# Optimization experiments

Hardware: AMD Instinct MI355X
Metric: run time of the kernel (lower is better)

The kernel has to match this reference:

```python
import jax, jax.numpy as jnp
import numpy as np
import math

H = 32      # num attention heads
KV = 8      # num key/value heads
D = 64      # head dim
ROPE_BASE = 10000.0


def _rope_cos_sin(seq_len, dtype):
    inv_freq = 1.0 / (ROPE_BASE ** (jnp.arange(0, D, 2, dtype=jnp.float32) / D))
    t = jnp.arange(seq_len, dtype=jnp.float32)
    freqs = jnp.einsum('i,j->ij', t, inv_freq)          # [S, D/2]
    emb = jnp.concatenate([freqs, freqs], axis=-1)       # [S, D]
    return jnp.cos(emb).astype(dtype)[None, None], jnp.sin(emb).astype(dtype)[None, None]


def _rotate_half(x):
    x1, x2 = x[..., : D // 2], x[..., D // 2:]
    return jnp.concatenate([-x2, x1], axis=-1)


def setup_inputs() -> dict:
    key = jax.random.key(0)
    ks = jax.random.split(key, 5)
    B, S, Hid = 1, 2048, 2048
    hidden_states = jax.random.normal(ks[0], (B, S, Hid), dtype=jnp.float32)
    Wq = jax.random.normal(ks[1], (Hid, H * D), dtype=jnp.float32) * (1.0 / math.sqrt(Hid))
    Wk = jax.random.normal(ks[2], (Hid, KV * D), dtype=jnp.float32) * (1.0 / math.sqrt(Hid))
    Wv = jax.random.normal(ks[3], (Hid, KV * D), dtype=jnp.float32) * (1.0 / math.sqrt(Hid))
    Wo = jax.random.normal(ks[4], (H * D, Hid), dtype=jnp.float32) * (1.0 / math.sqrt(H * D))
    # additive causal mask
    causal = jnp.tril(jnp.ones((S, S), dtype=bool))
    attention_mask = jnp.where(causal, 0.0, -1e9).astype(jnp.float32)[None, None]
    return {"hidden_states": hidden_states, "Wq": Wq, "Wk": Wk, "Wv": Wv,
            "Wo": Wo, "attention_mask": attention_mask}


def reference(hidden_states, Wq, Wk, Wv, Wo, attention_mask):
    B, S, _ = hidden_states.shape
    groups = H // KV
    # projections -> [B, heads, S, D]
    q = (hidden_states @ Wq).reshape(B, S, H, D).transpose(0, 2, 1, 3)
    k = (hidden_states @ Wk).reshape(B, S, KV, D).transpose(0, 2, 1, 3)
    v = (hidden_states @ Wv).reshape(B, S, KV, D).transpose(0, 2, 1, 3)
    # RoPE
    cos, sin = _rope_cos_sin(S, q.dtype)
    q = q * cos + _rotate_half(q) * sin
    k = k * cos + _rotate_half(k) * sin
    # GQA head expansion (repeat_interleave along head axis)
    k = jnp.repeat(k, groups, axis=1)
    v = jnp.repeat(v, groups, axis=1)
    # scaled dot-product attention (eager)
    scores = jnp.einsum('bhqd,bhkd->bhqk', q, k) / math.sqrt(D)
    scores = scores + attention_mask
    probs = jax.nn.softmax(scores.astype(jnp.float32), axis=-1).astype(q.dtype)
    attn = jnp.einsum('bhqk,bhkd->bhqd', probs, v)
    attn = attn.transpose(0, 2, 1, 3).reshape(B, S, H * D)
    return attn @ Wo
```

## Files before the change

### kernel.cpp

```cpp
#include <hip/hip_runtime.h>
#include <hip/hip_bf16.h>
#include <math.h>

#define S_LEN 2048
#define HID   2048
#define NH    32
#define NKV   8
#define HD    64
#define KVW   (NKV * HD)

typedef __attribute__((ext_vector_type(8))) short bf16x8;
typedef __attribute__((ext_vector_type(4))) float f32x4;
typedef unsigned short u16;

__device__ __forceinline__ u16 f2bf(float f) {
    return (u16)((__builtin_bit_cast(unsigned, f) + 0x8000u) >> 16);
}
__device__ __forceinline__ float bf2f(u16 v) {
    unsigned u = ((unsigned)v) << 16;
    return __builtin_bit_cast(float, u);
}
__device__ __forceinline__ unsigned pack2bf(float a, float b) {
    unsigned ua = __builtin_bit_cast(unsigned, a) + 0x8000u;
    unsigned ub = __builtin_bit_cast(unsigned, b) + 0x8000u;
    return (ua >> 16) | (ub & 0xFFFF0000u);
}
__device__ __forceinline__ void stage16(const u16* g, u16* lds_base) {
    __builtin_amdgcn_global_load_lds((const __attribute__((address_space(1))) void*)g,
                                     (__attribute__((address_space(3))) void*)lds_base, 16, 0, 0);
}

__global__ __launch_bounds__(256) void cvt_bf16x8_kernel(const float* __restrict__ X,
                                                         u16* __restrict__ Y, int n8) {
    int i = blockIdx.x * 256 + threadIdx.x;
    if (i >= n8) return;
    const float4* p = (const float4*)(X + (size_t)i * 8);
    float4 a = p[0], b = p[1];
    uint4 o;
    o.x = pack2bf(a.x, a.y);
    o.y = pack2bf(a.z, a.w);
    o.z = pack2bf(b.x, b.y);
    o.w = pack2bf(b.z, b.w);
    *(uint4*)(Y + (size_t)i * 8) = o;
}

__global__ __launch_bounds__(256) void transpose_cvt4(const float* __restrict__ Wq,
                                                      const float* __restrict__ Wk,
                                                      const float* __restrict__ Wv,
                                                      const float* __restrict__ Wo,
                                                      u16* __restrict__ WqkvT,
                                                      u16* __restrict__ WoT) {
    const float* X; u16* Y; int C;
    const int z = blockIdx.z;
    if (z == 0)      { X = Wq; Y = WqkvT;                        C = HID; }
    else if (z == 1) { X = Wo; Y = WoT;                          C = HID; }
    else if (z == 2) { X = Wk; Y = WqkvT + (size_t)2048 * HID;   C = KVW; }
    else             { X = Wv; Y = WqkvT + (size_t)2560 * HID;   C = KVW; }
    const int c0 = blockIdx.x * 32, r0 = blockIdx.y * 32;
    if (c0 >= C) return;
    __shared__ float T[32][33];
    const int tx = threadIdx.x & 31, ty = threadIdx.x >> 5;
#pragma unroll
    for (int i = 0; i < 4; i++)
        T[ty + 8 * i][tx] = X[(size_t)(r0 + ty + 8 * i) * C + c0 + tx];
    __syncthreads();
#pragma unroll
    for (int i = 0; i < 4; i++)
        Y[(size_t)(c0 + ty + 8 * i) * HID + r0 + tx] = f2bf(T[tx][ty + 8 * i]);
}

template <int EPI>
__global__ __launch_bounds__(256, 4) void gemm_bf16(const u16* __restrict__ A,
                                                    const u16* __restrict__ Bt,
                                                    float* __restrict__ C,
                                                    u16* __restrict__ Qh,
                                                    u16* __restrict__ Kh,
                                                    u16* __restrict__ Vt,
                                                    int K) {
    __shared__ u16 As[2][128 * 64];
    __shared__ u16 Bs[2][64 * 64];

    const int t = threadIdx.x;
    const int w = t >> 6, lane = t & 63;
    const int qd = lane >> 4, r = lane & 15;
    const int wm = w >> 1, wn = w & 1;
    const int bm = blockIdx.y * 128, bn = blockIdx.x * 64;
    const bool kblk = (EPI == 1) && (bn >= 2048) && (bn < 2560);

    f32x4 acc[4][2];
#pragma unroll
    for (int i = 0; i < 4; i++)
#pragma unroll
        for (int j = 0; j < 2; j++) {
            acc[i][j][0] = 0.f; acc[i][j][1] = 0.f; acc[i][j][2] = 0.f; acc[i][j][3] = 0.f;
        }

    auto stageA = [&](int k0, u16* dstA) {
#pragma unroll
        for (int rd = 0; rd < 4; rd++) {
            int chunk = rd * 4 + w;
            int tt = chunk >> 1, ss = chunk & 1;
            const u16* g = A + (size_t)(bm + tt * 16 + r) * K + k0 + ss * 32 + qd * 8;
            stage16(g, dstA + chunk * 512);
        }
    };
    auto stageB = [&](int k0, u16* dstB) {
#pragma unroll
        for (int rd = 0; rd < 2; rd++) {
            int chunk = rd * 4 + w;
            int tt = chunk >> 1, ss = chunk & 1;
            const u16* g = Bt + (size_t)(bn + tt * 16 + r) * K + k0 + ss * 32 + qd * 8;
            stage16(g, dstB + chunk * 512);
        }
    };

    stageA(0, As[0]);
    stageB(0, Bs[0]);
    __syncthreads();
    int cur = 0;

    for (int k0 = 0; k0 < K; k0 += 64) {
        if (k0 + 64 < K) {
            stageA(k0 + 64, As[cur ^ 1]);
            stageB(k0 + 64, Bs[cur ^ 1]);
        }

#pragma unroll
        for (int ss = 0; ss < 2; ss++) {
            bf16x8 af[4], bfr[2];
#pragma unroll
            for (int i = 0; i < 4; i++)
                af[i] = *(const bf16x8*)&As[cur][((wm * 4 + i) * 2 + ss) * 512 + lane * 8];
#pragma unroll
            for (int j = 0; j < 2; j++) {
                int tile = kblk ? (wn + 2 * j) : (wn * 2 + j);
                bfr[j] = *(const bf16x8*)&Bs[cur][(tile * 2 + ss) * 512 + lane * 8];
            }
#pragma unroll
            for (int i = 0; i < 4; i++)
#pragma unroll
                for (int j = 0; j < 2; j++)
                    acc[i][j] = __builtin_amdgcn_mfma_f32_16x16x32_bf16(af[i], bfr[j], acc[i][j], 0, 0, 0);
        }

        __syncthreads();
        cur ^= 1;
    }

    const int row0 = bm + wm * 64;
    if (EPI == 0) {
#pragma unroll
        for (int i = 0; i < 4; i++)
#pragma unroll
            for (int j = 0; j < 2; j++)
#pragma unroll
                for (int reg = 0; reg < 4; reg++)
                    C[(size_t)(row0 + i * 16 + qd * 4 + reg) * HID + bn + wn * 32 + j * 16 + r] =
                        acc[i][j][reg];
    } else if (bn < 2048) {
#pragma unroll
        for (int i = 0; i < 4; i++)
#pragma unroll
            for (int j = 0; j < 2; j++)
#pragma unroll
                for (int reg = 0; reg < 4; reg++)
                    Qh[(size_t)(row0 + i * 16 + qd * 4 + reg) * HID + bn + wn * 32 + j * 16 + r] =
                        f2bf(acc[i][j][reg]);
    } else if (kblk) {
        const int c0 = wn * 16 + r;
        const float inv = __expf(-(float)c0 * 0.2878231366242596f);
#pragma unroll
        for (int i = 0; i < 4; i++)
#pragma unroll
            for (int reg = 0; reg < 4; reg++) {
                int srow = row0 + i * 16 + qd * 4 + reg;
                float ang = (float)srow * inv;
                float cs = cosf(ang), sn = sinf(ang);
                float k1 = acc[i][0][reg], k2 = acc[i][1][reg];
                size_t o = (size_t)srow * KVW + (bn - 2048) + c0;
                Kh[o]      = f2bf(k1 * cs - k2 * sn);
                Kh[o + 32] = f2bf(k2 * cs + k1 * sn);
            }
    } else {
#pragma unroll
        for (int i = 0; i < 4; i++)
#pragma unroll
            for (int j = 0; j < 2; j++) {
                int nrel = (bn - 2560) + wn * 32 + j * 16 + r;
                int m0 = row0 + i * 16 + qd * 4;
                ushort4 v;
                v.x = f2bf(acc[i][j][0]); v.y = f2bf(acc[i][j][1]);
                v.z = f2bf(acc[i][j][2]); v.w = f2bf(acc[i][j][3]);
                *(ushort4*)(Vt + (size_t)nrel * S_LEN + m0) = v;
            }
    }
}

__global__ __launch_bounds__(512, 6) void attn_mfma(const u16* __restrict__ Qh,
                                                    const u16* __restrict__ K,
                                                    const u16* __restrict__ Vt,
                                                    u16* __restrict__ O) {
    __shared__ u16 Kbuf[2][4096];
    __shared__ u16 Vbuf[4096];
    __shared__ u16 P_lds[8][16][72];

    const int w    = threadIdx.x >> 6;
    const int lane = threadIdx.x & 63;
    const int qd   = lane >> 4;
    const int r    = lane & 15;
    const int qb   = 15 - (int)blockIdx.x;
    const int h    = blockIdx.y;
    const int kvh  = h >> 2;
    const int q0w  = qb * 128 + w * 16;

    const u16* qrow = Qh + (size_t)(q0w + r) * (NH * HD) + h * HD;
    bf16x8 qlo = *(const bf16x8*)(qrow + qd * 8);
    bf16x8 qhi = *(const bf16x8*)(qrow + 32 + qd * 8);
    float y1[8], y2[8];
    const float spos = (float)(q0w + r);
    const float LN1E4_OVER_32 = 0.2878231366242596f;
#pragma unroll
    for (int i = 0; i < 8; i++) {
        int jj = qd * 8 + i;
        float x1 = bf2f((u16)qlo[i]);
        float x2 = bf2f((u16)qhi[i]);
        float inv = __expf(-(float)jj * LN1E4_OVER_32);
        float ang = spos * inv;
        float c = cosf(ang), sn = sinf(ang);
        y1[i] = (x1 * c - x2 * sn) * 0.125f;
        y2[i] = (x2 * c + x1 * sn) * 0.125f;
    }
    bf16x8 qfrag[2];
    {
        union { unsigned u[4]; bf16x8 v; } a, b;
#pragma unroll
        for (int i = 0; i < 4; i++) {
            a.u[i] = pack2bf(y1[2 * i], y1[2 * i + 1]);
            b.u[i] = pack2bf(y2[2 * i], y2[2 * i + 1]);
        }
        qfrag[0] = a.v; qfrag[1] = b.v;
    }

    bf16x8 ones;
    {
        union { u16 s[8]; bf16x8 v; } u;
#pragma unroll
        for (int i = 0; i < 8; i++) u.s[i] = 0x3F80;
        ones = u.v;
    }

    f32x4 oacc[4];
    f32x4 lacc;
#pragma unroll
    for (int i = 0; i < 4; i++) { oacc[i][0]=0.f; oacc[i][1]=0.f; oacc[i][2]=0.f; oacc[i][3]=0.f; }
    lacc[0]=0.f; lacc[1]=0.f; lacc[2]=0.f; lacc[3]=0.f;

    const int ktmax = 2 * qb + 1;

#define STAGE_K(kt_, buf_)                                                        \
    {                                                                             \
        const u16* g = K + (size_t)((kt_) * 64 + (w >> 1) * 16 + r) * KVW         \
                         + kvh * HD + (w & 1) * 32 + qd * 8;                      \
        stage16(g, &Kbuf[buf_][w * 512]);                                         \
    }
#define STAGE_V(kt_)                                                              \
    {                                                                             \
        const u16* g = Vt + (size_t)(kvh * HD + (w >> 1) * 16 + r) * S_LEN        \
                          + (kt_) * 64 + (w & 1) * 32 + qd * 8;                   \
        stage16(g, &Vbuf[w * 512]);                                               \
    }

    STAGE_K(0, 0);
    __syncthreads();
    int cur = 0;

    for (int kt = 0; kt <= ktmax; kt++) {
        STAGE_V(kt);
        if (kt < ktmax) STAGE_K(kt + 1, cur ^ 1);

        f32x4 s[4];
#pragma unroll
        for (int nt = 0; nt < 4; nt++) {
            bf16x8 kf0 = *(const bf16x8*)&Kbuf[cur][(nt * 2 + 0) * 512 + lane * 8];
            bf16x8 kf1 = *(const bf16x8*)&Kbuf[cur][(nt * 2 + 1) * 512 + lane * 8];
            f32x4 z; z[0]=0.f; z[1]=0.f; z[2]=0.f; z[3]=0.f;
            z = __builtin_amdgcn_mfma_f32_16x16x32_bf16(qfrag[0], kf0, z, 0, 0, 0);
            s[nt] = __builtin_amdgcn_mfma_f32_16x16x32_bf16(qfrag[1], kf1, z, 0, 0, 0);
        }

        if (kt * 64 + 63 > q0w) {
#pragma unroll
            for (int nt = 0; nt < 4; nt++) {
                int key = kt * 64 + nt * 16 + r;
#pragma unroll
                for (int reg = 0; reg < 4; reg++) {
                    int qg = q0w + qd * 4 + reg;
                    if (key > qg) s[nt][reg] = -1e30f;
                }
            }
        }

#pragma unroll
        for (int nt = 0; nt < 4; nt++)
#pragma unroll
            for (int reg = 0; reg < 4; reg++)
                P_lds[w][qd * 4 + reg][nt * 16 + r] = f2bf(__expf(s[nt][reg]));

        __syncthreads();

#pragma unroll
        for (int c = 0; c < 2; c++) {
            bf16x8 pf = *(const bf16x8*)&P_lds[w][r][c * 32 + qd * 8];
            lacc = __builtin_amdgcn_mfma_f32_16x16x32_bf16(pf, ones, lacc, 0, 0, 0);
#pragma unroll
            for (int ntd = 0; ntd < 4; ntd++) {
                bf16x8 vf = *(const bf16x8*)&Vbuf[(ntd * 2 + c) * 512 + lane * 8];
                oacc[ntd] = __builtin_amdgcn_mfma_f32_16x16x32_bf16(pf, vf, oacc[ntd], 0, 0, 0);
            }
        }

        __syncthreads();
        cur ^= 1;
    }
#undef STAGE_K
#undef STAGE_V

    float rl[4];
#pragma unroll
    for (int reg = 0; reg < 4; reg++) rl[reg] = 1.f / lacc[reg];
#pragma unroll
    for (int ntd = 0; ntd < 4; ntd++)
#pragma unroll
        for (int reg = 0; reg < 4; reg++)
            O[(size_t)(q0w + qd * 4 + reg) * (NH * HD) + h * HD + ntd * 16 + r] =
                f2bf(oacc[ntd][reg] * rl[reg]);
}

extern "C" void kernel_launch(void* const* d_in, const int* in_sizes, int n_in,
                              void* d_out, int out_size, void* d_ws, size_t ws_size,
                              hipStream_t stream) {
    const float* hidden = (const float*)d_in[0];
    const float* Wq = (const float*)d_in[1];
    const float* Wk = (const float*)d_in[2];
    const float* Wv = (const float*)d_in[3];
    const float* Wo = (const float*)d_in[4];
    float* out = (float*)d_out;

    char* ws = (char*)d_ws;
    const size_t MB = 1024 * 1024;
    u16* Hh     = (u16*)(ws + 0 * MB);
    u16* WqkvT  = (u16*)(ws + 8 * MB);
    u16* WoT    = (u16*)(ws + 20 * MB);
    u16* Qh     = (u16*)(ws + 28 * MB);
    u16* Kh     = (u16*)(ws + 36 * MB);
    u16* Vt     = (u16*)(ws + 38 * MB);
    u16* Ob     = WqkvT;

    cvt_bf16x8_kernel<<<(S_LEN * HID / 8 + 255) / 256, 256, 0, stream>>>(hidden, Hh, S_LEN * HID / 8);
    transpose_cvt4<<<dim3(HID / 32, HID / 32, 4), 256, 0, stream>>>(Wq, Wk, Wv, Wo, WqkvT, WoT);

    gemm_bf16<1><<<dim3(3072 / 64, S_LEN / 128), 256, 0, stream>>>(Hh, WqkvT, nullptr, Qh, Kh, Vt, HID);

    attn_mfma<<<dim3(S_LEN / 128, NH), 512, 0, stream>>>(Qh, Kh, Vt, Ob);

    gemm_bf16<0><<<dim3(HID / 64, S_LEN / 128), 256, 0, stream>>>(Ob, WoT, out, nullptr, nullptr, nullptr, HID);
}
```

Baseline: 286.1 us.

## Widen GEMM tiles to 128x128 and double-buffer V in attention

The bf16 GEMM moves from 128x64 tiles with 4 waves to 128x128 tiles with 8 waves. A and B are now staged together, one 16-row strip per wave, and the RoPE epilogue remaps so each block covers two K heads. This raises reuse of the A tile, but it halves the number of blocks on a 256-CU GPU, which risks load imbalance and lower occupancy. In attention, V is now double-buffered and prefetched alongside K, and the barrier between the per-wave P write and P read is removed, cutting one workgroup sync per key tile.

After: 285.0 us. Within noise of the previous version (-0.4%).

```diff
diff --git a/kernel.cpp b/kernel.cpp
--- a/kernel.cpp
+++ b/kernel.cpp
@@ -70,7 +70,7 @@
 }
 
 template <int EPI>
-__global__ __launch_bounds__(256, 4) void gemm_bf16(const u16* __restrict__ A,
+__global__ __launch_bounds__(512, 4) void gemm_bf16(const u16* __restrict__ A,
                                                     const u16* __restrict__ Bt,
                                                     float* __restrict__ C,
                                                     u16* __restrict__ Qh,
@@ -78,13 +78,13 @@
                                                     u16* __restrict__ Vt,
                                                     int K) {
     __shared__ u16 As[2][128 * 64];
-    __shared__ u16 Bs[2][64 * 64];
+    __shared__ u16 Bs[2][128 * 64];
 
     const int t = threadIdx.x;
     const int w = t >> 6, lane = t & 63;
     const int qd = lane >> 4, r = lane & 15;
-    const int wm = w >> 1, wn = w & 1;
-    const int bm = blockIdx.y * 128, bn = blockIdx.x * 64;
+    const int wm = w >> 2, wn = w & 3;
+    const int bm = blockIdx.y * 128, bn = blockIdx.x * 128;
     const bool kblk = (EPI == 1) && (bn >= 2048) && (bn < 2560);
 
     f32x4 acc[4][2];
@@ -95,35 +95,23 @@
             acc[i][j][0] = 0.f; acc[i][j][1] = 0.f; acc[i][j][2] = 0.f; acc[i][j][3] = 0.f;
         }
 
-    auto stageA = [&](int k0, u16* dstA) {
-#pragma unroll
-        for (int rd = 0; rd < 4; rd++) {
-            int chunk = rd * 4 + w;
-            int tt = chunk >> 1, ss = chunk & 1;
-            const u16* g = A + (size_t)(bm + tt * 16 + r) * K + k0 + ss * 32 + qd * 8;
-            stage16(g, dstA + chunk * 512);
+    auto stageAB = [&](int k0, u16* dstA, u16* dstB) {
+#pragma unroll
+        for (int rd = 0; rd < 2; rd++) {
+            const u16* ga = A + (size_t)(bm + w * 16 + r) * K + k0 + rd * 32 + qd * 8;
+            stage16(ga, dstA + (w * 2 + rd) * 512);
+            const u16* gb = Bt + (size_t)(bn + w * 16 + r) * K + k0 + rd * 32 + qd * 8;
+            stage16(gb, dstB + (w * 2 + rd) * 512);
         }
     };
-    auto stageB = [&](int k0, u16* dstB) {
-#pragma unroll
-        for (int rd = 0; rd < 2; rd++) {
-            int chunk = rd * 4 + w;
-            int tt = chunk >> 1, ss = chunk & 1;
-            const u16* g = Bt + (size_t)(bn + tt * 16 + r) * K + k0 + ss * 32 + qd * 8;
-            stage16(g, dstB + chunk * 512);
-        }
-    };
-
-    stageA(0, As[0]);
-    stageB(0, Bs[0]);
+
+    stageAB(0, As[0], Bs[0]);
     __syncthreads();
     int cur = 0;
 
     for (int k0 = 0; k0 < K; k0 += 64) {
-        if (k0 + 64 < K) {
-            stageA(k0 + 64, As[cur ^ 1]);
-            stageB(k0 + 64, Bs[cur ^ 1]);
-        }
+        if (k0 + 64 < K)
+            stageAB(k0 + 64, As[cur ^ 1], Bs[cur ^ 1]);
 
 #pragma unroll
         for (int ss = 0; ss < 2; ss++) {
@@ -133,7 +121,7 @@
                 af[i] = *(const bf16x8*)&As[cur][((wm * 4 + i) * 2 + ss) * 512 + lane * 8];
 #pragma unroll
             for (int j = 0; j < 2; j++) {
-                int tile = kblk ? (wn + 2 * j) : (wn * 2 + j);
+                int tile = kblk ? ((wn >> 1) * 4 + (wn & 1) + 2 * j) : (wn * 2 + j);
                 bfr[j] = *(const bf16x8*)&Bs[cur][(tile * 2 + ss) * 512 + lane * 8];
             }
 #pragma unroll
@@ -167,7 +155,8 @@
                     Qh[(size_t)(row0 + i * 16 + qd * 4 + reg) * HID + bn + wn * 32 + j * 16 + r] =
                         f2bf(acc[i][j][reg]);
     } else if (kblk) {
-        const int c0 = wn * 16 + r;
+        const int c0 = (wn & 1) * 16 + r;
+        const int hb = (bn - 2048) + (wn >> 1) * 64;
         const float inv = __expf(-(float)c0 * 0.2878231366242596f);
 #pragma unroll
         for (int i = 0; i < 4; i++)
@@ -177,7 +166,7 @@
                 float ang = (float)srow * inv;
                 float cs = cosf(ang), sn = sinf(ang);
                 float k1 = acc[i][0][reg], k2 = acc[i][1][reg];
-                size_t o = (size_t)srow * KVW + (bn - 2048) + c0;
+                size_t o = (size_t)srow * KVW + hb + c0;
                 Kh[o]      = f2bf(k1 * cs - k2 * sn);
                 Kh[o + 32] = f2bf(k2 * cs + k1 * sn);
             }
@@ -201,7 +190,7 @@
                                                     const u16* __restrict__ Vt,
                                                     u16* __restrict__ O) {
     __shared__ u16 Kbuf[2][4096];
-    __shared__ u16 Vbuf[4096];
+    __shared__ u16 Vbuf[2][4096];
     __shared__ u16 P_lds[8][16][72];
 
     const int w    = threadIdx.x >> 6;
@@ -263,20 +252,23 @@
                          + kvh * HD + (w & 1) * 32 + qd * 8;                      \
         stage16(g, &Kbuf[buf_][w * 512]);                                         \
     }
-#define STAGE_V(kt_)                                                              \
+#define STAGE_V(kt_, buf_)                                                        \
     {                                                                             \
         const u16* g = Vt + (size_t)(kvh * HD + (w >> 1) * 16 + r) * S_LEN        \
                           + (kt_) * 64 + (w & 1) * 32 + qd * 8;                   \
-        stage16(g, &Vbuf[w * 512]);                                               \
+        stage16(g, &Vbuf[buf_][w * 512]);                                         \
     }
 
     STAGE_K(0, 0);
+    STAGE_V(0, 0);
     __syncthreads();
     int cur = 0;
 
     for (int kt = 0; kt <= ktmax; kt++) {
-        STAGE_V(kt);
-        if (kt < ktmax) STAGE_K(kt + 1, cur ^ 1);
+        if (kt < ktmax) {
+            STAGE_K(kt + 1, cur ^ 1);
+            STAGE_V(kt + 1, cur ^ 1);
+        }
 
         f32x4 s[4];
 #pragma unroll
@@ -306,7 +298,6 @@
             for (int reg = 0; reg < 4; reg++)
                 P_lds[w][qd * 4 + reg][nt * 16 + r] = f2bf(__expf(s[nt][reg]));
 
-        __syncthreads();
 
 #pragma unroll
         for (int c = 0; c < 2; c++) {
@@ -314,7 +305,7 @@
             lacc = __builtin_amdgcn_mfma_f32_16x16x32_bf16(pf, ones, lacc, 0, 0, 0);
 #pragma unroll
             for (int ntd = 0; ntd < 4; ntd++) {
-                bf16x8 vf = *(const bf16x8*)&Vbuf[(ntd * 2 + c) * 512 + lane * 8];
+                bf16x8 vf = *(const bf16x8*)&Vbuf[cur][(ntd * 2 + c) * 512 + lane * 8];
                 oacc[ntd] = __builtin_amdgcn_mfma_f32_16x16x32_bf16(pf, vf, oacc[ntd], 0, 0, 0);
             }
         }
@@ -359,9 +350,9 @@
     cvt_bf16x8_kernel<<<(S_LEN * HID / 8 + 255) / 256, 256, 0, stream>>>(hidden, Hh, S_LEN * HID / 8);
     transpose_cvt4<<<dim3(HID / 32, HID / 32, 4), 256, 0, stream>>>(Wq, Wk, Wv, Wo, WqkvT, WoT);
 
-    gemm_bf16<1><<<dim3(3072 / 64, S_LEN / 128), 256, 0, stream>>>(Hh, WqkvT, nullptr, Qh, Kh, Vt, HID);
+    gemm_bf16<1><<<dim3(3072 / 128, S_LEN / 128), 512, 0, stream>>>(Hh, WqkvT, nullptr, Qh, Kh, Vt, HID);
 
     attn_mfma<<<dim3(S_LEN / 128, NH), 512, 0, stream>>>(Qh, Kh, Vt, Ob);
 
-    gemm_bf16<0><<<dim3(HID / 64, S_LEN / 128), 256, 0, stream>>>(Ob, WoT, out, nullptr, nullptr, nullptr, HID);
-}
+    gemm_bf16<0><<<dim3(HID / 128, S_LEN / 128), 512, 0, stream>>>(Ob, WoT, out, nullptr, nullptr, nullptr, HID);
+}
```
